# Optimization experiments

Hardware: AMD Instinct MI355X
Metric: run time of the kernel (lower is better)

## Reference

```python
import jax, jax.numpy as jnp
import numpy as np

DIM = 50
K = 51  # kernel_size == DIM + 1 (required by the original view())
E = 6   # num_elems
NT = 29 # num_targets
B = 8
DN = ('NCDHW', 'OIDHW', 'NCDHW')


def setup_inputs() -> dict:
    key = jax.random.key(0)
    ks = jax.random.split(key, 14)
    f = jnp.float32
    inp = {
        'x': jax.random.uniform(ks[0], (B, E, DIM, DIM, DIM), dtype=f),
        'sigma': 3.0 * jnp.ones((E,), dtype=f),
        'w1': jax.random.normal(ks[1], (32, E, 3, 3, 3), dtype=f) * 0.1,
        'b1': jnp.full((32,), 0.01, dtype=f),
        'w2': jax.random.normal(ks[2], (64, 32, 3, 3, 3), dtype=f) * 0.05,
        'b2': jnp.full((64,), 0.01, dtype=f),
        'w3': jax.random.normal(ks[3], (128, 64, 3, 3, 3), dtype=f) * 0.05,
        'b3': jnp.full((128,), 0.01, dtype=f),
        'w4': jax.random.normal(ks[4], (256, 128, 3, 3, 3), dtype=f) * 0.03,
        'b4': jnp.full((256,), 0.01, dtype=f),
        'fw1': jax.random.normal(ks[5], (128, 256), dtype=f) * 0.06,
        'fb1': jnp.full((128,), 0.01, dtype=f),
        'fw2': jax.random.normal(ks[6], (NT, 128), dtype=f) * 0.08,
        'fb2': jnp.full((NT,), 0.01, dtype=f),
    }
    return inp


def _blur_kernel(sigma):
    # Gauss transformation kernel, shape (E, 1, K, K, K)
    c = jnp.arange(K, dtype=jnp.float32)
    mean = (K - 1) / 2.0
    d2 = (c - mean) ** 2
    # squared radius grid (K,K,K), symmetric so the torch transpose(3,0) axis swap is a no-op
    r2 = d2[:, None, None] + d2[None, :, None] + d2[None, None, :]
    var = sigma ** 2  # (E,)
    a = 1.0 / (2.0 * np.pi * var)  # (E,)
    kern = a[:, None, None, None] * jnp.exp(-r2[None] / (2.0 * var)[:, None, None, None])
    kern = kern / jnp.sum(kern)  # normalize by GLOBAL sum (as in torch code)
    return kern[:, None]  # (E,1,K,K,K)


def _conv3(x, w, b):
    y = jax.lax.conv_general_dilated(x, w, (1, 1, 1), 'VALID', dimension_numbers=DN)
    return y + b[None, :, None, None, None]


def _pool(x):
    return jax.lax.reduce_window(x, -jnp.inf, jax.lax.max,
                                 (1, 1, 2, 2, 2), (1, 1, 2, 2, 2), 'VALID')


def reference(x, sigma, w1, b1, w2, b2, w3, b3, w4, b4, fw1, fb1, fw2, fb2):
    # blur: grouped 3D conv with on-the-fly Gaussian kernel, padding 25 keeps DIM
    kern = _blur_kernel(sigma)
    pad = (K - 1) // 2
    xc = jax.lax.conv_general_dilated(x, kern, (1, 1, 1), [(pad, pad)] * 3,
                                      feature_group_count=E, dimension_numbers=DN)
    xc = xc / jnp.max(xc)
    # conv stack: (conv -> pool -> relu) x4
    h = jax.nn.relu(_pool(_conv3(xc, w1, b1)))   # (B,32,24,24,24)
    h = jax.nn.relu(_pool(_conv3(h, w2, b2)))    # (B,64,11,11,11)
    h = jax.nn.relu(_pool(_conv3(h, w3, b3)))    # (B,128,4,4,4)
    h = jax.nn.relu(_pool(_conv3(h, w4, b4)))    # (B,256,1,1,1)
    v = h.reshape(x.shape[0], -1)                # (B,256)
    y1 = jax.nn.relu(v @ fw1.T + fb1)
    return y1 @ fw2.T + fb2                      # (B,29)
```

## Files before the change

kernel.cpp:

```cpp
#include <hip/hip_runtime.h>
#include <math.h>

#define DIMX 50
#define KK   51
#define NE   6
#define NB   8
#define NVOX ((size_t)NB * NE * DIMX * DIMX * DIMX)

typedef short bf16x8 __attribute__((ext_vector_type(8)));
typedef float f32x4  __attribute__((ext_vector_type(4)));

__device__ __forceinline__ unsigned short f2bf(float f) {
    unsigned u = __float_as_uint(f);
    u += 0x7fffu + ((u >> 16) & 1u);
    return (unsigned short)(u >> 16);
}
__device__ __forceinline__ float bf2f(unsigned short h) {
    return __uint_as_float((unsigned)h << 16);
}
__device__ __forceinline__ uint4 pack8(const unsigned short v[8]) {
    uint4 q;
    q.x = v[0] | ((unsigned)v[1] << 16);
    q.y = v[2] | ((unsigned)v[3] << 16);
    q.z = v[4] | ((unsigned)v[5] << 16);
    q.w = v[6] | ((unsigned)v[7] << 16);
    return q;
}
__device__ __forceinline__ int offA(int o, int k) {
    return ((((o >> 4) * 2 + (k >> 5)) * 64 + ((k >> 3) & 3) * 16 + (o & 15)) << 3) + (k & 7);
}

__global__ void taps_kernel(const float* __restrict__ sigma,
                            unsigned short* __restrict__ MA, unsigned short* __restrict__ MB,
                            float* __restrict__ maxval) {
    __shared__ float sg[NE * KK];
    __shared__ float sgs[NE * KK];
    __shared__ float ssum[NE];
    int t = threadIdx.x;
    if (t == 0) *maxval = 0.f;
    if (t < NE * KK) {
        int e = t / KK, i = t % KK;
        float d = (float)i - 25.0f;
        float var = sigma[e] * sigma[e];
        sg[t] = expf(-d * d / (2.f * var));
    }
    __syncthreads();
    if (t < NE) {
        float s = 0.f;
        for (int i = 0; i < KK; ++i) s += sg[t * KK + i];
        ssum[t] = s;
    }
    __syncthreads();
    if (t < NE * KK) {
        int e = t / KK;
        float S = 0.f;
        for (int e2 = 0; e2 < NE; ++e2) {
            float var2 = sigma[e2] * sigma[e2];
            float a2 = 1.f / (2.f * (float)M_PI * var2);
            float se = ssum[e2];
            S += a2 * se * se * se;
        }
        float var = sigma[e] * sigma[e];
        float a = 1.f / (2.f * (float)M_PI * var);
        sgs[t] = sg[t] * (a / S);
    }
    __syncthreads();
    const int TOT = 2 * 6 * 4 * 2 * 64 * 8;
    for (int i = t; i < 2 * TOT; i += 512) {
        int which = i / TOT;
        int r = i % TOT;
        int q = r;
        int j = q & 7; q >>= 3;
        int l = q & 63; q >>= 6;
        int kc = q & 1; q >>= 1;
        int tile = q & 3; q >>= 2;
        int e = q % 6; q /= 6;
        int hl = q;
        int own = tile * 16 + (l & 15);
        int k   = kc * 32 + ((l >> 4) << 3) + j;
        float v = 0.f;
        if (own < 50 && k < 50) {
            int d = k - own + 25;
            if (d >= 0 && d < KK) v = (which == 0 ? sg : sgs)[e * KK + d];
        }
        unsigned short h = f2bf(v);
        unsigned short out = (hl == 0) ? h : f2bf(v - bf2f(h));
        (which == 0 ? MA : MB)[r] = out;
    }
}

__global__ __launch_bounds__(64)
void blur_k1(const float* __restrict__ in, float* __restrict__ W1,
             const unsigned short* __restrict__ MA) {
    __shared__ unsigned short Bhi[4096], Blo[4096];
    const int l = threadIdx.x, lm = l & 15, lg = l >> 4;
    const int y = blockIdx.x % 50, be = blockIdx.x / 50, e = be % 6;
    const float* pb = in + (size_t)be * 125000 + y * 50;
#pragma unroll
    for (int xt = 0; xt < 4; ++xt)
#pragma unroll
        for (int kc = 0; kc < 2; ++kc) {
            const int xx = xt * 16 + lm;
            unsigned short vh[8], vl[8];
#pragma unroll
            for (int j = 0; j < 8; ++j) {
                int z = kc * 32 + lg * 8 + j;
                float v = (z < 50 && xx < 50) ? pb[(size_t)z * 2500 + xx] : 0.f;
                unsigned short h = f2bf(v);
                vh[j] = h; vl[j] = f2bf(v - bf2f(h));
            }
            const int T = xt * 2 + kc;
            *(uint4*)(Bhi + (T * 64 + l) * 8) = pack8(vh);
            *(uint4*)(Blo + (T * 64 + l) * 8) = pack8(vl);
        }
    __builtin_amdgcn_wave_barrier();
    asm volatile("s_waitcnt lgkmcnt(0)" ::: "memory");
    __builtin_amdgcn_sched_barrier(0);
    float* ob = W1 + (size_t)be * 125000 + y * 50;
    const f32x4 z4 = {0.f, 0.f, 0.f, 0.f};
#pragma unroll 1
    for (int ozt = 0; ozt < 4; ++ozt) {
        bf16x8 Ah[2], Al[2];
#pragma unroll
        for (int kc = 0; kc < 2; ++kc) {
            Ah[kc] = *(const bf16x8*)(MA + (((size_t)(0 * 6 + e) * 4 + ozt) * 2 + kc) * 512 + l * 8);
            Al[kc] = *(const bf16x8*)(MA + (((size_t)(1 * 6 + e) * 4 + ozt) * 2 + kc) * 512 + l * 8);
        }
#pragma unroll
        for (int xt = 0; xt < 4; ++xt) {
            f32x4 acc = z4;
#pragma unroll
            for (int kc = 0; kc < 2; ++kc) {
                bf16x8 bh = *(const bf16x8*)(Bhi + ((xt * 2 + kc) * 64 + l) * 8);
                bf16x8 bl = *(const bf16x8*)(Blo + ((xt * 2 + kc) * 64 + l) * 8);
                acc = __builtin_amdgcn_mfma_f32_16x16x32_bf16(Ah[kc], bh, acc, 0, 0, 0);
                acc = __builtin_amdgcn_mfma_f32_16x16x32_bf16(Ah[kc], bl, acc, 0, 0, 0);
                acc = __builtin_amdgcn_mfma_f32_16x16x32_bf16(Al[kc], bh, acc, 0, 0, 0);
            }
            int xx = xt * 16 + lm;
            if (xx < 50) {
#pragma unroll
                for (int i = 0; i < 4; ++i) {
                    int oz = ozt * 16 + lg * 4 + i;
                    if (oz < 50) ob[(size_t)oz * 2500 + xx] = acc[i];
                }
            }
        }
    }
}

__global__ __launch_bounds__(64)
void blur_k2(float* __restrict__ W1, const unsigned short* __restrict__ MA,
             const unsigned short* __restrict__ MB, float* __restrict__ maxval) {
    __shared__ unsigned short Bhi[4096], Blo[4096];
    const int l = threadIdx.x, lm = l & 15, lg = l >> 4;
    const int z = blockIdx.x % 50, be = blockIdx.x / 50, e = be % 6;
    float* pb = W1 + (size_t)be * 125000 + (size_t)z * 2500;
#pragma unroll
    for (int xt = 0; xt < 4; ++xt)
#pragma unroll
        for (int kc = 0; kc < 2; ++kc) {
            const int xx = xt * 16 + lm;
            unsigned short vh[8], vl[8];
#pragma unroll
            for (int j = 0; j < 8; ++j) {
                int yy = kc * 32 + lg * 8 + j;
                float v = (yy < 50 && xx < 50) ? pb[yy * 50 + xx] : 0.f;
                unsigned short h = f2bf(v);
                vh[j] = h; vl[j] = f2bf(v - bf2f(h));
            }
            const int T = xt * 2 + kc;
            *(uint4*)(Bhi + (T * 64 + l) * 8) = pack8(vh);
            *(uint4*)(Blo + (T * 64 + l) * 8) = pack8(vl);
        }
    __builtin_amdgcn_wave_barrier();
    asm volatile("s_waitcnt lgkmcnt(0)" ::: "memory");
    __builtin_amdgcn_sched_barrier(0);
    const f32x4 z4 = {0.f, 0.f, 0.f, 0.f};
    f32x4 accQ[4][4];
#pragma unroll
    for (int oyt = 0; oyt < 4; ++oyt) {
        bf16x8 Ah[2], Al[2];
#pragma unroll
        for (int kc = 0; kc < 2; ++kc) {
            Ah[kc] = *(const bf16x8*)(MA + (((size_t)(0 * 6 + e) * 4 + oyt) * 2 + kc) * 512 + l * 8);
            Al[kc] = *(const bf16x8*)(MA + (((size_t)(1 * 6 + e) * 4 + oyt) * 2 + kc) * 512 + l * 8);
        }
#pragma unroll
        for (int xt = 0; xt < 4; ++xt) {
            f32x4 acc = z4;
#pragma unroll
            for (int kc = 0; kc < 2; ++kc) {
                bf16x8 bh = *(const bf16x8*)(Bhi + ((xt * 2 + kc) * 64 + l) * 8);
                bf16x8 bl = *(const bf16x8*)(Blo + ((xt * 2 + kc) * 64 + l) * 8);
                acc = __builtin_amdgcn_mfma_f32_16x16x32_bf16(Ah[kc], bh, acc, 0, 0, 0);
                acc = __builtin_amdgcn_mfma_f32_16x16x32_bf16(Ah[kc], bl, acc, 0, 0, 0);
                acc = __builtin_amdgcn_mfma_f32_16x16x32_bf16(Al[kc], bh, acc, 0, 0, 0);
            }
            accQ[oyt][xt] = acc;
        }
    }
    __builtin_amdgcn_wave_barrier();
    asm volatile("s_waitcnt lgkmcnt(0)" ::: "memory");
    __builtin_amdgcn_sched_barrier(0);
#pragma unroll
    for (int oyt = 0; oyt < 4; ++oyt)
#pragma unroll
        for (int xt = 0; xt < 4; ++xt)
#pragma unroll
            for (int i = 0; i < 4; ++i) {
                int oy = oyt * 16 + lg * 4 + i;
                int xx = xt * 16 + lm;
                float qv = accQ[oyt][xt][i];
                unsigned short h = f2bf(qv);
                int off = offA(oy, xx);
                Bhi[off] = h; Blo[off] = f2bf(qv - bf2f(h));
            }
    __builtin_amdgcn_wave_barrier();
    asm volatile("s_waitcnt lgkmcnt(0)" ::: "memory");
    __builtin_amdgcn_sched_barrier(0);
    float mmax = 0.f;
#pragma unroll 1
    for (int oyt = 0; oyt < 4; ++oyt) {
        bf16x8 Qh[2], Ql[2];
#pragma unroll
        for (int kc = 0; kc < 2; ++kc) {
            Qh[kc] = *(const bf16x8*)(Bhi + ((oyt * 2 + kc) * 64 + l) * 8);
            Ql[kc] = *(const bf16x8*)(Blo + ((oyt * 2 + kc) * 64 + l) * 8);
        }
#pragma unroll
        for (int oxt = 0; oxt < 4; ++oxt) {
            f32x4 acc = z4;
#pragma unroll
            for (int kc = 0; kc < 2; ++kc) {
                bf16x8 mh = *(const bf16x8*)(MB + (((size_t)(0 * 6 + e) * 4 + oxt) * 2 + kc) * 512 + l * 8);
                bf16x8 ml = *(const bf16x8*)(MB + (((size_t)(1 * 6 + e) * 4 + oxt) * 2 + kc) * 512 + l * 8);
                acc = __builtin_amdgcn_mfma_f32_16x16x32_bf16(Qh[kc], mh, acc, 0, 0, 0);
                acc = __builtin_amdgcn_mfma_f32_16x16x32_bf16(Qh[kc], ml, acc, 0, 0, 0);
                acc = __builtin_amdgcn_mfma_f32_16x16x32_bf16(Ql[kc], mh, acc, 0, 0, 0);
            }
            int ox = oxt * 16 + lm;
            if (ox < 50) {
#pragma unroll
                for (int i = 0; i < 4; ++i) {
                    int oy = oyt * 16 + lg * 4 + i;
                    if (oy < 50) {
                        float r = acc[i];
                        pb[oy * 50 + ox] = r;
                        mmax = fmaxf(mmax, r);
                    }
                }
            }
        }
    }
    for (int o = 32; o; o >>= 1) mmax = fmaxf(mmax, __shfl_xor(mmax, o));
    if (l == 0) atomicMax((int*)maxval, __float_as_int(mmax));
}

__global__ __launch_bounds__(256)
void t1_kernel(const float* __restrict__ A, unsigned short* __restrict__ X1) {
    const int z = blockIdx.x % 50, b = blockIdx.x / 50;
    const float* ab = A + (size_t)b * 6 * 125000 + (size_t)z * 2500;
    unsigned short* xb = X1 + ((size_t)b * 125000 + (size_t)z * 2500) * 8;
    for (int i = threadIdx.x; i < 2500; i += 256) {
        unsigned short v[6];
#pragma unroll
        for (int e = 0; e < 6; ++e) v[e] = f2bf(ab[(size_t)e * 125000 + i]);
        uint4 q;
        q.x = v[0] | ((unsigned)v[1] << 16);
        q.y = v[2] | ((unsigned)v[3] << 16);
        q.z = v[4] | ((unsigned)v[5] << 16);
        q.w = 0u;
        *(uint4*)(xb + (size_t)i * 8) = q;
    }
}

__global__ void wprep_kernel(const float* __restrict__ W, unsigned short* __restrict__ out,
                             int CIN, int NCH, int NCOG) {
    int idx = blockIdx.x * 256 + threadIdx.x;
    int total = NCOG * 27 * NCH * 64;
    if (idx >= total) return;
    int l = idx & 63;
    int r = idx >> 6;
    int ch = r % NCH; r /= NCH;
    int tap = r % 27;
    int cog = r / 27;
    int co = cog * 16 + (l & 15);
    unsigned short v[8];
#pragma unroll
    for (int j = 0; j < 8; ++j) {
        int ci = ch * 32 + (l >> 4) * 8 + j;
        v[j] = (ci < CIN) ? f2bf(W[((size_t)co * CIN + ci) * 27 + tap]) : (unsigned short)0;
    }
    uint4 q;
    q.x = v[0] | ((unsigned)v[1] << 16);
    q.y = v[2] | ((unsigned)v[3] << 16);
    q.z = v[4] | ((unsigned)v[5] << 16);
    q.w = v[6] | ((unsigned)v[7] << 16);
    ((uint4*)out)[idx] = q;
}

__global__ void wprep1_kernel(const float* __restrict__ W, unsigned short* __restrict__ out) {
    int idx = blockIdx.x * 64 + threadIdx.x;
    if (idx >= 2 * 9 * 64) return;
    int l = idx & 63;
    int r = idx >> 6;
    int tg = r % 9;
    int cog = r / 9;
    int xsel = l >> 4;
    int co = cog * 16 + (l & 15);
    unsigned short v[8];
#pragma unroll
    for (int j = 0; j < 8; ++j) {
        float wv = 0.f;
        if (j < 6 && xsel < 3) wv = W[((size_t)co * 6 + j) * 27 + tg * 3 + xsel];
        v[j] = f2bf(wv);
    }
    uint4 q;
    q.x = v[0] | ((unsigned)v[1] << 16);
    q.y = v[2] | ((unsigned)v[3] << 16);
    q.z = v[4] | ((unsigned)v[5] << 16);
    q.w = v[6] | ((unsigned)v[7] << 16);
    ((uint4*)out)[idx] = q;
}

__global__ __launch_bounds__(64, 3)
void conv1_mfma(const unsigned short* __restrict__ X8, const unsigned short* __restrict__ wp1,
                const float* __restrict__ bias, const float* __restrict__ maxval,
                unsigned short* __restrict__ X2) {
    const int l = threadIdx.x, lm = l & 15, lg = l >> 4;
    const int q = (int)(gridDim.x >> 3);
    const int bid = ((int)blockIdx.x & 7) * q + ((int)blockIdx.x >> 3);
    const int s0 = bid * 8;
    const int r0 = s0 / 72;
    const int cog = r0 % 2;
    const int pz  = (r0 / 2) % 24;
    const int b   = r0 / 48;
    uint4 B9[9];
    const uint4* wpb = (const uint4*)wp1 + cog * 9 * 64;
#pragma unroll
    for (int t = 0; t < 9; ++t) B9[t] = wpb[t * 64 + l];
    const float rmv = 1.0f / (*maxval);
    const float bia = bias[cog * 16 + lm];
    const unsigned short* Xb = X8 + (size_t)b * 125000 * 8;
    const f32x4 z4 = {0.f, 0.f, 0.f, 0.f};
#pragma unroll 1
    for (int si = 0; si < 8; ++si) {
        const int sid = s0 + si;
        const int xs = sid % 3;
        const int py = (sid / 3) % 24;
        const int x0 = xs * 16;
        f32x4 acc[2][2];
#pragma unroll
        for (int cz = 0; cz < 2; ++cz)
#pragma unroll
            for (int cy = 0; cy < 2; ++cy) acc[cz][cy] = z4;
#pragma unroll
        for (int zi = 0; zi < 4; ++zi) {
            const int zin = 2 * pz + zi;
#pragma unroll
            for (int yi = 0; yi < 4; ++yi) {
                const int yin = 2 * py + yi;
                const unsigned short* rowb = Xb + (size_t)(zin * 50 + yin) * 50 * 8;
                bf16x8 a = *(const bf16x8*)(rowb + (x0 + lm + lg) * 8);
#pragma unroll
                for (int cz = 0; cz < 2; ++cz) {
                    const int kz = zi - cz;
                    if (kz < 0 || kz > 2) continue;
#pragma unroll
                    for (int cy = 0; cy < 2; ++cy) {
                        const int ky = yi - cy;
                        if (ky < 0 || ky > 2) continue;
                        acc[cz][cy] = __builtin_amdgcn_mfma_f32_16x16x32_bf16(
                            a, *(const bf16x8*)&B9[kz * 3 + ky], acc[cz][cy], 0, 0, 0);
                    }
                }
            }
        }
        const int co = cog * 16 + lm;
#pragma unroll
        for (int ip = 0; ip < 2; ++ip) {
            float m0 = fmaxf(fmaxf(acc[0][0][2 * ip], acc[0][1][2 * ip]),
                             fmaxf(acc[1][0][2 * ip], acc[1][1][2 * ip]));
            float m1 = fmaxf(fmaxf(acc[0][0][2 * ip + 1], acc[0][1][2 * ip + 1]),
                             fmaxf(acc[1][0][2 * ip + 1], acc[1][1][2 * ip + 1]));
            float o = fmaxf(fmaxf(m0, m1) * rmv + bia, 0.f);
            int px = x0 / 2 + lg * 2 + ip;
            X2[((((size_t)b * 24 + pz) * 24 + py) * 24 + px) * 32 + co] = f2bf(o);
        }
    }
}

template <int DIN, int DP, int CI, int NCH, int NCOG, int NPY, int NXS, int SPB, int NPZ>
__global__ __launch_bounds__(64, 3)
void convN_mfma(const unsigned short* __restrict__ X, const unsigned short* __restrict__ wp,
                const float* __restrict__ bias, unsigned short* __restrict__ Y, int COUT) {
    const int l = threadIdx.x, lm = l & 15, lg = l >> 4;
    const int qq = (int)(gridDim.x >> 3);
    const int bid = ((int)blockIdx.x & 7) * qq + ((int)blockIdx.x >> 3);
    const int s0 = bid * SPB;
    const int r0 = s0 / (NPY * NXS);
    const int cog = r0 % NCOG;
    const int pz  = (r0 / NCOG) % NPZ;
    const int b   = r0 / (NCOG * NPZ);
    const float bia = bias[cog * 16 + lm];
    const unsigned short* Xb = X + (size_t)b * DIN * DIN * DIN * CI;
    const uint4* wp4 = (const uint4*)wp;
    const f32x4 z4 = {0.f, 0.f, 0.f, 0.f};
#pragma unroll 1
    for (int si = 0; si < SPB; ++si) {
        const int sid = s0 + si;
        const int xs = sid % NXS;
        const int py = (sid / NXS) % NPY;
        const int x0 = xs * 16;
        int xo[3];
#pragma unroll
        for (int kx = 0; kx < 3; ++kx) {
            int xin = x0 + kx + lm;
            if (xin > DIN - 1) xin = DIN - 1;
            xo[kx] = xin * CI + lg * 8;
        }
        f32x4 acc[2][2];
#pragma unroll
        for (int cz = 0; cz < 2; ++cz)
#pragma unroll
            for (int cy = 0; cy < 2; ++cy) acc[cz][cy] = z4;
#pragma unroll 1
        for (int ch = 0; ch < NCH; ++ch) {
            uint4 B[27];
            const uint4* wpb = wp4 + ((size_t)cog * 27 * NCH + ch) * 64;
#pragma unroll
            for (int t = 0; t < 27; ++t) B[t] = wpb[(size_t)t * NCH * 64 + l];
            const unsigned short* Xc = Xb + ch * 32;
#pragma unroll
            for (int zi = 0; zi < 4; ++zi) {
                const int zin = 2 * pz + zi;
#pragma unroll
                for (int yi = 0; yi < 4; ++yi) {
                    const int yin = 2 * py + yi;
                    const unsigned short* rowb = Xc + (size_t)(zin * DIN + yin) * DIN * CI;
#pragma unroll
                    for (int kx = 0; kx < 3; ++kx) {
                        bf16x8 a = *(const bf16x8*)(rowb + xo[kx]);
#pragma unroll
                        for (int cz = 0; cz < 2; ++cz) {
                            const int kz = zi - cz;
                            if (kz < 0 || kz > 2) continue;
#pragma unroll
                            for (int cy = 0; cy < 2; ++cy) {
                                const int ky = yi - cy;
                                if (ky < 0 || ky > 2) continue;
                                const int tap = (kz * 3 + ky) * 3 + kx;
                                acc[cz][cy] = __builtin_amdgcn_mfma_f32_16x16x32_bf16(
                                    a, *(const bf16x8*)&B[tap], acc[cz][cy], 0, 0, 0);
                            }
                        }
                    }
                }
            }
        }
        const int co = cog * 16 + lm;
#pragma unroll
        for (int ip = 0; ip < 2; ++ip) {
            float m0 = fmaxf(fmaxf(acc[0][0][2 * ip], acc[0][1][2 * ip]),
                             fmaxf(acc[1][0][2 * ip], acc[1][1][2 * ip]));
            float m1 = fmaxf(fmaxf(acc[0][0][2 * ip + 1], acc[0][1][2 * ip + 1]),
                             fmaxf(acc[1][0][2 * ip + 1], acc[1][1][2 * ip + 1]));
            float o = fmaxf(fmaxf(m0, m1) + bia, 0.f);
            int px = x0 / 2 + lg * 2 + ip;
            if (px < DP)
                Y[((((size_t)b * DP + pz) * DP + py) * DP + px) * COUT + co] = f2bf(o);
        }
    }
}

__global__ void conv4_kernel(const unsigned short* __restrict__ X4, const float* __restrict__ w,
                             const float* __restrict__ bias, float* __restrict__ out) {
    int wid = (int)((blockIdx.x * blockDim.x + threadIdx.x) >> 6);
    int lane = threadIdx.x & 63;
    if (wid >= NB * 256) return;
    int b = wid >> 8, co = wid & 255;
    float acc[8];
#pragma unroll
    for (int i = 0; i < 8; ++i) acc[i] = 0.f;
    for (int half = 0; half < 2; ++half) {
        int ci = lane + half * 64;
        float win[64];
#pragma unroll
        for (int v = 0; v < 64; ++v)
            win[v] = bf2f(X4[((size_t)b * 64 + v) * 128 + ci]);
        const float* wc = w + ((size_t)co * 128 + ci) * 27;
        float wr[27];
#pragma unroll
        for (int i = 0; i < 27; ++i) wr[i] = wc[i];
#pragma unroll
        for (int kz = 0; kz < 3; ++kz)
#pragma unroll
            for (int ky = 0; ky < 3; ++ky)
#pragma unroll
                for (int kx = 0; kx < 3; ++kx) {
                    float wv = wr[(kz * 3 + ky) * 3 + kx];
#pragma unroll
                    for (int oz = 0; oz < 2; ++oz)
#pragma unroll
                        for (int oy = 0; oy < 2; ++oy)
#pragma unroll
                            for (int ox = 0; ox < 2; ++ox)
                                acc[(oz * 2 + oy) * 2 + ox] =
                                    fmaf(wv, win[((oz + kz) * 4 + (oy + ky)) * 4 + ox + kx],
                                         acc[(oz * 2 + oy) * 2 + ox]);
                }
    }
#pragma unroll
    for (int o = 32; o; o >>= 1)
#pragma unroll
        for (int i = 0; i < 8; ++i) acc[i] += __shfl_xor(acc[i], o);
    if (lane == 0) {
        float m = acc[0];
#pragma unroll
        for (int i = 1; i < 8; ++i) m = fmaxf(m, acc[i]);
        out[(size_t)b * 256 + co] = fmaxf(m + bias[co], 0.f);
    }
}

__global__ void head_kernel(const float* __restrict__ v,
                            const float* __restrict__ fw1, const float* __restrict__ fb1,
                            const float* __restrict__ fw2, const float* __restrict__ fb2,
                            float* __restrict__ out) {
    int b = blockIdx.x, t = threadIdx.x;
    __shared__ float sv[256];
    __shared__ float s1[128];
    sv[t] = v[b * 256 + t];
    sv[t + 128] = v[b * 256 + t + 128];
    __syncthreads();
    float acc = fb1[t];
    const float* wr = fw1 + t * 256;
    for (int k = 0; k < 256; ++k) acc = fmaf(wr[k], sv[k], acc);
    s1[t] = fmaxf(acc, 0.f);
    __syncthreads();
    if (t < 29) {
        float a2 = fb2[t];
        const float* w2 = fw2 + t * 128;
        for (int k = 0; k < 128; ++k) a2 = fmaf(w2[k], s1[k], a2);
        out[b * 29 + t] = a2;
    }
}

extern "C" void kernel_launch(void* const* d_in, const int* in_sizes, int n_in,
                              void* d_out, int out_size, void* d_ws, size_t ws_size,
                              hipStream_t stream) {
    const float* x     = (const float*)d_in[0];
    const float* sigma = (const float*)d_in[1];
    const float* w1    = (const float*)d_in[2];
    const float* b1    = (const float*)d_in[3];
    const float* w2    = (const float*)d_in[4];
    const float* b2    = (const float*)d_in[5];
    const float* w3    = (const float*)d_in[6];
    const float* b3    = (const float*)d_in[7];
    const float* w4    = (const float*)d_in[8];
    const float* b4    = (const float*)d_in[9];
    const float* fw1   = (const float*)d_in[10];
    const float* fb1   = (const float*)d_in[11];
    const float* fw2   = (const float*)d_in[12];
    const float* fb2   = (const float*)d_in[13];
    float* out = (float*)d_out;

    float* W1 = (float*)d_ws;
    unsigned short* X1  = (unsigned short*)(W1 + NVOX);
    unsigned short* X2  = X1 + 8000064;
    unsigned short* X3  = X2 + 3538944;
    unsigned short* X4  = X3 + 681472;
    unsigned short* wp1 = X4 + 65536;
    unsigned short* wp2 = wp1 + 9216;
    unsigned short* wp3 = wp2 + 55296;
    unsigned short* MA  = wp3 + 221184;
    unsigned short* MB  = MA + 49152;
    float* mx = (float*)(MB + 49152);
    float* v4 = mx + 1;

    taps_kernel<<<1, 512, 0, stream>>>(sigma, MA, MB, mx);

    blur_k1<<<NB * NE * 50, 64, 0, stream>>>(x, W1, MA);
    blur_k2<<<NB * NE * 50, 64, 0, stream>>>(W1, MA, MB, mx);

    t1_kernel<<<400, 256, 0, stream>>>(W1, X1);
    wprep1_kernel<<<18, 64, 0, stream>>>(w1, wp1);
    wprep_kernel<<<27, 256, 0, stream>>>(w2, wp2, 32, 1, 4);
    wprep_kernel<<<108, 256, 0, stream>>>(w3, wp3, 64, 2, 8);

    conv1_mfma<<<3456, 64, 0, stream>>>(X1, wp1, b1, mx, X2);
    convN_mfma<24, 11, 32, 1, 4, 11, 2, 2, 11><<<3872, 64, 0, stream>>>(X2, wp2, b2, X3, 64);
    convN_mfma<11, 4, 64, 2, 8, 4, 1, 1, 4><<<1024, 64, 0, stream>>>(X3, wp3, b3, X4, 128);

    conv4_kernel<<<512, 256, 0, stream>>>(X4, w4, b4, v4);
    head_kernel<<<8, 128, 0, stream>>>(v4, fw1, fb1, fw2, fb2, out);
}
```

Baseline: 212.2 us.

## Fuse bf16 channel-interleave into blur_k2 and keep blur operands in registers

blur_k2 now writes its output straight into the bf16 channel-interleaved X1 buffer, so the separate t1_kernel transpose pass and the fp32 write-back of the second blur stage are removed. It also swizzles block order so the six channels of a voxel plane are processed on nearby blocks. Both blur kernels now keep the hi/lo bf16 input fragments in registers instead of staging them through LDS, with blur_k1 hoisting all tap matrices up front. The trade-off is higher register pressure and strided 2-byte scattered stores into X1 instead of packed 16-byte stores.

```diff
diff --git a/kernel.cpp b/kernel.cpp
--- a/kernel.cpp
+++ b/kernel.cpp
@@ -92,15 +92,25 @@
 __global__ __launch_bounds__(64)
 void blur_k1(const float* __restrict__ in, float* __restrict__ W1,
              const unsigned short* __restrict__ MA) {
-    __shared__ unsigned short Bhi[4096], Blo[4096];
     const int l = threadIdx.x, lm = l & 15, lg = l >> 4;
     const int y = blockIdx.x % 50, be = blockIdx.x / 50, e = be % 6;
     const float* pb = in + (size_t)be * 125000 + y * 50;
-#pragma unroll
-    for (int xt = 0; xt < 4; ++xt)
+    bf16x8 Ah[4][2], Al[4][2];
+#pragma unroll
+    for (int ozt = 0; ozt < 4; ++ozt)
 #pragma unroll
         for (int kc = 0; kc < 2; ++kc) {
-            const int xx = xt * 16 + lm;
+            Ah[ozt][kc] = *(const bf16x8*)(MA + (((size_t)(0 * 6 + e) * 4 + ozt) * 2 + kc) * 512 + l * 8);
+            Al[ozt][kc] = *(const bf16x8*)(MA + (((size_t)(1 * 6 + e) * 4 + ozt) * 2 + kc) * 512 + l * 8);
+        }
+    float* ob = W1 + (size_t)be * 125000 + y * 50;
+    const f32x4 z4 = {0.f, 0.f, 0.f, 0.f};
+#pragma unroll 1
+    for (int xt = 0; xt < 4; ++xt) {
+        const int xx = xt * 16 + lm;
+        bf16x8 bh[2], bl[2];
+#pragma unroll
+        for (int kc = 0; kc < 2; ++kc) {
             unsigned short vh[8], vl[8];
 #pragma unroll
             for (int j = 0; j < 8; ++j) {
@@ -109,58 +119,48 @@
                 unsigned short h = f2bf(v);
                 vh[j] = h; vl[j] = f2bf(v - bf2f(h));
             }
-            const int T = xt * 2 + kc;
-            *(uint4*)(Bhi + (T * 64 + l) * 8) = pack8(vh);
-            *(uint4*)(Blo + (T * 64 + l) * 8) = pack8(vl);
-        }
-    __builtin_amdgcn_wave_barrier();
-    asm volatile("s_waitcnt lgkmcnt(0)" ::: "memory");
-    __builtin_amdgcn_sched_barrier(0);
-    float* ob = W1 + (size_t)be * 125000 + y * 50;
-    const f32x4 z4 = {0.f, 0.f, 0.f, 0.f};
-#pragma unroll 1
-    for (int ozt = 0; ozt < 4; ++ozt) {
-        bf16x8 Ah[2], Al[2];
-#pragma unroll
-        for (int kc = 0; kc < 2; ++kc) {
-            Ah[kc] = *(const bf16x8*)(MA + (((size_t)(0 * 6 + e) * 4 + ozt) * 2 + kc) * 512 + l * 8);
-            Al[kc] = *(const bf16x8*)(MA + (((size_t)(1 * 6 + e) * 4 + ozt) * 2 + kc) * 512 + l * 8);
-        }
-#pragma unroll
-        for (int xt = 0; xt < 4; ++xt) {
-            f32x4 acc = z4;
+            uint4 qh = pack8(vh), ql = pack8(vl);
+            bh[kc] = *(bf16x8*)&qh; bl[kc] = *(bf16x8*)&ql;
+        }
+        f32x4 acc[4];
+#pragma unroll
+        for (int ozt = 0; ozt < 4; ++ozt) acc[ozt] = z4;
+#pragma unroll
+        for (int ozt = 0; ozt < 4; ++ozt)
 #pragma unroll
             for (int kc = 0; kc < 2; ++kc) {
-                bf16x8 bh = *(const bf16x8*)(Bhi + ((xt * 2 + kc) * 64 + l) * 8);
-                bf16x8 bl = *(const bf16x8*)(Blo + ((xt * 2 + kc) * 64 + l) * 8);
-                acc = __builtin_amdgcn_mfma_f32_16x16x32_bf16(Ah[kc], bh, acc, 0, 0, 0);
-                acc = __builtin_amdgcn_mfma_f32_16x16x32_bf16(Ah[kc], bl, acc, 0, 0, 0);
-                acc = __builtin_amdgcn_mfma_f32_16x16x32_bf16(Al[kc], bh, acc, 0, 0, 0);
-            }
-            int xx = xt * 16 + lm;
-            if (xx < 50) {
+                acc[ozt] = __builtin_amdgcn_mfma_f32_16x16x32_bf16(Ah[ozt][kc], bh[kc], acc[ozt], 0, 0, 0);
+                acc[ozt] = __builtin_amdgcn_mfma_f32_16x16x32_bf16(Ah[ozt][kc], bl[kc], acc[ozt], 0, 0, 0);
+                acc[ozt] = __builtin_amdgcn_mfma_f32_16x16x32_bf16(Al[ozt][kc], bh[kc], acc[ozt], 0, 0, 0);
+            }
+        if (xx < 50) {
+#pragma unroll
+            for (int ozt = 0; ozt < 4; ++ozt)
 #pragma unroll
                 for (int i = 0; i < 4; ++i) {
                     int oz = ozt * 16 + lg * 4 + i;
-                    if (oz < 50) ob[(size_t)oz * 2500 + xx] = acc[i];
+                    if (oz < 50) ob[(size_t)oz * 2500 + xx] = acc[ozt][i];
                 }
-            }
         }
     }
 }
 
 __global__ __launch_bounds__(64)
-void blur_k2(float* __restrict__ W1, const unsigned short* __restrict__ MA,
-             const unsigned short* __restrict__ MB, float* __restrict__ maxval) {
-    __shared__ unsigned short Bhi[4096], Blo[4096];
+void blur_k2(const float* __restrict__ W1, const unsigned short* __restrict__ MA,
+             const unsigned short* __restrict__ MB, unsigned short* __restrict__ X1,
+             float* __restrict__ maxval) {
+    __shared__ unsigned short Qhi[4096], Qlo[4096];
     const int l = threadIdx.x, lm = l & 15, lg = l >> 4;
-    const int z = blockIdx.x % 50, be = blockIdx.x / 50, e = be % 6;
-    float* pb = W1 + (size_t)be * 125000 + (size_t)z * 2500;
-#pragma unroll
-    for (int xt = 0; xt < 4; ++xt)
+    const int q8 = (int)(gridDim.x >> 3);
+    const int logical = ((int)blockIdx.x & 7) * q8 + ((int)blockIdx.x >> 3);
+    const int e = logical % 6, bz = logical / 6, z = bz % 50, b = bz / 50;
+    const float* pb = W1 + (size_t)(b * 6 + e) * 125000 + (size_t)z * 2500;
+    bf16x8 Bh[4][2], Bl[4][2];
+#pragma unroll
+    for (int xt = 0; xt < 4; ++xt) {
+        const int xx = xt * 16 + lm;
 #pragma unroll
         for (int kc = 0; kc < 2; ++kc) {
-            const int xx = xt * 16 + lm;
             unsigned short vh[8], vl[8];
 #pragma unroll
             for (int j = 0; j < 8; ++j) {
@@ -169,16 +169,12 @@
                 unsigned short h = f2bf(v);
                 vh[j] = h; vl[j] = f2bf(v - bf2f(h));
             }
-            const int T = xt * 2 + kc;
-            *(uint4*)(Bhi + (T * 64 + l) * 8) = pack8(vh);
-            *(uint4*)(Blo + (T * 64 + l) * 8) = pack8(vl);
-        }
-    __builtin_amdgcn_wave_barrier();
-    asm volatile("s_waitcnt lgkmcnt(0)" ::: "memory");
-    __builtin_amdgcn_sched_barrier(0);
+            uint4 qh = pack8(vh), ql = pack8(vl);
+            Bh[xt][kc] = *(bf16x8*)&qh; Bl[xt][kc] = *(bf16x8*)&ql;
+        }
+    }
     const f32x4 z4 = {0.f, 0.f, 0.f, 0.f};
-    f32x4 accQ[4][4];
-#pragma unroll
+#pragma unroll 1
     for (int oyt = 0; oyt < 4; ++oyt) {
         bf16x8 Ah[2], Al[2];
 #pragma unroll
@@ -191,42 +187,33 @@
             f32x4 acc = z4;
 #pragma unroll
             for (int kc = 0; kc < 2; ++kc) {
-                bf16x8 bh = *(const bf16x8*)(Bhi + ((xt * 2 + kc) * 64 + l) * 8);
-                bf16x8 bl = *(const bf16x8*)(Blo + ((xt * 2 + kc) * 64 + l) * 8);
-                acc = __builtin_amdgcn_mfma_f32_16x16x32_bf16(Ah[kc], bh, acc, 0, 0, 0);
-                acc = __builtin_amdgcn_mfma_f32_16x16x32_bf16(Ah[kc], bl, acc, 0, 0, 0);
-                acc = __builtin_amdgcn_mfma_f32_16x16x32_bf16(Al[kc], bh, acc, 0, 0, 0);
-            }
-            accQ[oyt][xt] = acc;
-        }
-    }
-    __builtin_amdgcn_wave_barrier();
-    asm volatile("s_waitcnt lgkmcnt(0)" ::: "memory");
-    __builtin_amdgcn_sched_barrier(0);
-#pragma unroll
-    for (int oyt = 0; oyt < 4; ++oyt)
-#pragma unroll
-        for (int xt = 0; xt < 4; ++xt)
+                acc = __builtin_amdgcn_mfma_f32_16x16x32_bf16(Ah[kc], Bh[xt][kc], acc, 0, 0, 0);
+                acc = __builtin_amdgcn_mfma_f32_16x16x32_bf16(Ah[kc], Bl[xt][kc], acc, 0, 0, 0);
+                acc = __builtin_amdgcn_mfma_f32_16x16x32_bf16(Al[kc], Bh[xt][kc], acc, 0, 0, 0);
+            }
 #pragma unroll
             for (int i = 0; i < 4; ++i) {
                 int oy = oyt * 16 + lg * 4 + i;
                 int xx = xt * 16 + lm;
-                float qv = accQ[oyt][xt][i];
+                float qv = acc[i];
                 unsigned short h = f2bf(qv);
                 int off = offA(oy, xx);
-                Bhi[off] = h; Blo[off] = f2bf(qv - bf2f(h));
-            }
+                Qhi[off] = h; Qlo[off] = f2bf(qv - bf2f(h));
+            }
+        }
+    }
     __builtin_amdgcn_wave_barrier();
     asm volatile("s_waitcnt lgkmcnt(0)" ::: "memory");
     __builtin_amdgcn_sched_barrier(0);
     float mmax = 0.f;
+    unsigned short* xb = X1 + ((size_t)b * 125000 + (size_t)z * 2500) * 8 + e;
 #pragma unroll 1
     for (int oyt = 0; oyt < 4; ++oyt) {
         bf16x8 Qh[2], Ql[2];
 #pragma unroll
         for (int kc = 0; kc < 2; ++kc) {
-            Qh[kc] = *(const bf16x8*)(Bhi + ((oyt * 2 + kc) * 64 + l) * 8);
-            Ql[kc] = *(const bf16x8*)(Blo + ((oyt * 2 + kc) * 64 + l) * 8);
+            Qh[kc] = *(const bf16x8*)(Qhi + ((oyt * 2 + kc) * 64 + l) * 8);
+            Ql[kc] = *(const bf16x8*)(Qlo + ((oyt * 2 + kc) * 64 + l) * 8);
         }
 #pragma unroll
         for (int oxt = 0; oxt < 4; ++oxt) {
@@ -246,7 +233,7 @@
                     int oy = oyt * 16 + lg * 4 + i;
                     if (oy < 50) {
                         float r = acc[i];
-                        pb[oy * 50 + ox] = r;
+                        xb[((size_t)oy * 50 + ox) * 8] = f2bf(r);
                         mmax = fmaxf(mmax, r);
                     }
                 }
@@ -255,24 +242,6 @@
     }
     for (int o = 32; o; o >>= 1) mmax = fmaxf(mmax, __shfl_xor(mmax, o));
     if (l == 0) atomicMax((int*)maxval, __float_as_int(mmax));
-}
-
-__global__ __launch_bounds__(256)
-void t1_kernel(const float* __restrict__ A, unsigned short* __restrict__ X1) {
-    const int z = blockIdx.x % 50, b = blockIdx.x / 50;
-    const float* ab = A + (size_t)b * 6 * 125000 + (size_t)z * 2500;
-    unsigned short* xb = X1 + ((size_t)b * 125000 + (size_t)z * 2500) * 8;
-    for (int i = threadIdx.x; i < 2500; i += 256) {
-        unsigned short v[6];
-#pragma unroll
-        for (int e = 0; e < 6; ++e) v[e] = f2bf(ab[(size_t)e * 125000 + i]);
-        uint4 q;
-        q.x = v[0] | ((unsigned)v[1] << 16);
-        q.y = v[2] | ((unsigned)v[3] << 16);
-        q.z = v[4] | ((unsigned)v[5] << 16);
-        q.w = 0u;
-        *(uint4*)(xb + (size_t)i * 8) = q;
-    }
 }
 
 __global__ void wprep_kernel(const float* __restrict__ W, unsigned short* __restrict__ out,
@@ -292,12 +261,7 @@
         int ci = ch * 32 + (l >> 4) * 8 + j;
         v[j] = (ci < CIN) ? f2bf(W[((size_t)co * CIN + ci) * 27 + tap]) : (unsigned short)0;
     }
-    uint4 q;
-    q.x = v[0] | ((unsigned)v[1] << 16);
-    q.y = v[2] | ((unsigned)v[3] << 16);
-    q.z = v[4] | ((unsigned)v[5] << 16);
-    q.w = v[6] | ((unsigned)v[7] << 16);
-    ((uint4*)out)[idx] = q;
+    ((uint4*)out)[idx] = pack8(v);
 }
 
 __global__ void wprep1_kernel(const float* __restrict__ W, unsigned short* __restrict__ out) {
@@ -316,12 +280,7 @@
         if (j < 6 && xsel < 3) wv = W[((size_t)co * 6 + j) * 27 + tg * 3 + xsel];
         v[j] = f2bf(wv);
     }
-    uint4 q;
-    q.x = v[0] | ((unsigned)v[1] << 16);
-    q.y = v[2] | ((unsigned)v[3] << 16);
-    q.z = v[4] | ((unsigned)v[5] << 16);
-    q.w = v[6] | ((unsigned)v[7] << 16);
-    ((uint4*)out)[idx] = q;
+    ((uint4*)out)[idx] = pack8(v);
 }
 
 __global__ __launch_bounds__(64, 3)
@@ -581,9 +540,8 @@
     taps_kernel<<<1, 512, 0, stream>>>(sigma, MA, MB, mx);
 
     blur_k1<<<NB * NE * 50, 64, 0, stream>>>(x, W1, MA);
-    blur_k2<<<NB * NE * 50, 64, 0, stream>>>(W1, MA, MB, mx);
-
-    t1_kernel<<<400, 256, 0, stream>>>(W1, X1);
+    blur_k2<<<NB * NE * 50, 64, 0, stream>>>(W1, MA, MB, X1, mx);
+
     wprep1_kernel<<<18, 64, 0, stream>>>(w1, wp1);
     wprep_kernel<<<27, 256, 0, stream>>>(w2, wp2, 32, 1, 4);
     wprep_kernel<<<108, 256, 0, stream>>>(w3, wp3, 64, 2, 8);
```

Result: faster. 205.5 us (-3.2%).
